# Kernel tuning notes

Measured on AMD Instinct MI355X. Metric: run time of the kernel, lower is better.

The kernel has to match this reference:

```python
import jax, jax.numpy as jnp
import numpy as np

B, S, H = 16, 2048, 1024


def setup_inputs() -> dict:
    key = jax.random.key(0)
    ks = jax.random.split(key, 8)
    scale = 1.0 / np.sqrt(H)
    return {
        "seq_embeddings": jax.random.normal(ks[0], (B, S, H), dtype=jnp.float32),
        "mask": jax.random.randint(ks[1], (B, S), 0, 2, dtype=jnp.int32),
        "Wq": jax.random.normal(ks[2], (H, H), dtype=jnp.float32) * scale,
        "bq": jnp.zeros((H,), dtype=jnp.float32),
        "Wk": jax.random.normal(ks[3], (H, H), dtype=jnp.float32) * scale,
        "bk": jnp.zeros((H,), dtype=jnp.float32),
        "Wv": jax.random.normal(ks[4], (H, H), dtype=jnp.float32) * scale,
        "bv": jnp.zeros((H,), dtype=jnp.float32),
    }


def reference(seq_embeddings, mask, Wq, bq, Wk, bk, Wv, bv):
    # Linear layers (torch convention: x @ W.T + b)
    Q = jnp.einsum("bsh,oh->bso", seq_embeddings, Wq) + bq
    K = jnp.einsum("bsh,oh->bso", seq_embeddings, Wk) + bk
    V = jnp.einsum("bsh,oh->bso", seq_embeddings, Wv) + bv

    inv_sqrt_d = 1.0 / jnp.sqrt(jnp.asarray(Q.shape[-1], Q.dtype))
    scores = jnp.einsum("bqh,bkh->bqk", Q, K) * inv_sqrt_d  # [B,S,S]
    # mask keys: mask[b,k]==0 -> -1e9 additive-equivalent fill
    scores = jnp.where(mask[:, None, :] == 0, jnp.asarray(-1e9, scores.dtype), scores)
    weights = jax.nn.softmax(scores, axis=-1)
    output = jnp.einsum("bqk,bkh->bqh", weights, V)
    # zero out padded query positions
    output = jnp.where(mask[:, :, None] == 0, jnp.asarray(0.0, output.dtype), output)
    return output
```

## Files before the change

### kernel.cpp

```cpp
#include <hip/hip_runtime.h>

#define Bn 16
#define Sn 2048
#define Hn 1024

typedef float floatx4 __attribute__((ext_vector_type(4)));
typedef __bf16 bf16x8 __attribute__((ext_vector_type(8)));
typedef unsigned short ushort8v __attribute__((ext_vector_type(8)));
typedef unsigned short ushort4v __attribute__((ext_vector_type(4)));

__device__ __forceinline__ unsigned short f2bf(float f) {
  unsigned u = __builtin_bit_cast(unsigned, f);
  u += 0x7FFFu + ((u >> 16) & 1u);
  return (unsigned short)(u >> 16);
}

__device__ __forceinline__ void async16(const unsigned short* g, unsigned short* l) {
  typedef __attribute__((address_space(1))) const unsigned char gu8;
  typedef __attribute__((address_space(3))) unsigned char lu8;
  __builtin_amdgcn_global_load_lds((gu8*)g, (lu8*)l, 16, 0, 0);
}

__device__ __forceinline__ void gemm256(const unsigned short* __restrict__ Ab,
                                        const unsigned short* __restrict__ Bb,
                                        int lda, int ldb, int K,
                                        unsigned short* lds, floatx4 acc[8][4]) {
  const int t = threadIdx.x;
  const int l = t & 63;
  const int w = t >> 6;
  const int srow = ((t >> 7) << 4) | (t & 15);
  const int sk = ((t >> 4) & 7) << 3;
  const int la = ((l >> 4) << 7) | ((l & 15) << 3);
  const int NT = K >> 6;
  const int wm = w >> 2, wn = w & 3;

#pragma unroll
  for (int i = 0; i < 8; ++i)
#pragma unroll
    for (int j = 0; j < 4; ++j)
#pragma unroll
      for (int e = 0; e < 4; ++e) acc[i][j][e] = 0.f;

#define STAGE(dstbase, srcp, ld, kk)                                     \
  {                                                                      \
    const unsigned short* _s = (srcp) + (size_t)srow * (ld) + (kk) + sk; \
    unsigned short* _d = (dstbase) + t * 8;                              \
    async16(_s, _d);                                                     \
    async16(_s + (size_t)64 * (ld), _d + 4096);                          \
  }

  {
    const int k1 = (NT > 1 ? 1 : 0) << 6;
    STAGE(lds + 0, Ab, lda, 0);
    STAGE(lds + 8192, Ab + (size_t)128 * lda, lda, 0);
    STAGE(lds + 16384, Bb, ldb, 0);
    STAGE(lds + 24576, Bb + (size_t)128 * ldb, ldb, 0);
    STAGE(lds + 32768 + 16384, Bb, ldb, k1);
    STAGE(lds + 32768 + 24576, Bb + (size_t)128 * ldb, ldb, k1);
  }
  asm volatile("s_waitcnt vmcnt(4)" ::: "memory");
  __builtin_amdgcn_s_barrier();
  __builtin_amdgcn_sched_barrier(0);

  bf16x8 aq[4][2], bA[2][2], bB[2][2];

  for (int tt = 0; tt < NT; ++tt) {
    unsigned short* bufc = lds + (tt & 1) * 32768;
    unsigned short* bufn = lds + ((tt & 1) ^ 1) * 32768;
    const unsigned short* As = bufc + wm * 8192;
    const unsigned short* Bs = bufc + 16384 + (wn >> 1) * 8192;
    const int cb = (wn & 1) * 4;
    const int kA = (tt + 1 < NT ? tt + 1 : 0) << 6;
    const int kB = (tt + 2 < NT ? tt + 2 : 0) << 6;

#pragma unroll
    for (int rf = 0; rf < 4; ++rf)
#pragma unroll
      for (int ks = 0; ks < 2; ++ks)
        aq[rf][ks] = *(const bf16x8*)(const void*)(As + rf * 1024 + ks * 512 + la);
#pragma unroll
    for (int cf = 0; cf < 2; ++cf)
#pragma unroll
      for (int ks = 0; ks < 2; ++ks)
        bA[cf][ks] = *(const bf16x8*)(const void*)(Bs + (cb + cf) * 1024 + ks * 512 + la);
    STAGE(bufn, Ab, lda, kA);
    __builtin_amdgcn_s_barrier();
    asm volatile("s_waitcnt lgkmcnt(0)" ::: "memory");
    __builtin_amdgcn_sched_barrier(0);
    __builtin_amdgcn_s_setprio(1);
#pragma unroll
    for (int rf = 0; rf < 4; ++rf)
#pragma unroll
      for (int cf = 0; cf < 2; ++cf)
#pragma unroll
        for (int ks = 0; ks < 2; ++ks)
          acc[rf][cf] = __builtin_amdgcn_mfma_f32_16x16x32_bf16(aq[rf][ks], bA[cf][ks], acc[rf][cf], 0, 0, 0);
    __builtin_amdgcn_s_setprio(0);
    __builtin_amdgcn_sched_barrier(0);
    __builtin_amdgcn_s_barrier();
    __builtin_amdgcn_sched_barrier(0);

#pragma unroll
    for (int cf = 0; cf < 2; ++cf)
#pragma unroll
      for (int ks = 0; ks < 2; ++ks)
        bB[cf][ks] = *(const bf16x8*)(const void*)(Bs + (cb + 2 + cf) * 1024 + ks * 512 + la);
    STAGE(bufn + 8192, Ab + (size_t)128 * lda, lda, kA);
    __builtin_amdgcn_s_barrier();
    asm volatile("s_waitcnt lgkmcnt(0)" ::: "memory");
    __builtin_amdgcn_sched_barrier(0);
    __builtin_amdgcn_s_setprio(1);
#pragma unroll
    for (int rf = 0; rf < 4; ++rf)
#pragma unroll
      for (int cf = 0; cf < 2; ++cf)
#pragma unroll
        for (int ks = 0; ks < 2; ++ks)
          acc[rf][2 + cf] = __builtin_amdgcn_mfma_f32_16x16x32_bf16(aq[rf][ks], bB[cf][ks], acc[rf][2 + cf], 0, 0, 0);
    __builtin_amdgcn_s_setprio(0);
    __builtin_amdgcn_sched_barrier(0);
    __builtin_amdgcn_s_barrier();
    __builtin_amdgcn_sched_barrier(0);

#pragma unroll
    for (int rf = 0; rf < 4; ++rf)
#pragma unroll
      for (int ks = 0; ks < 2; ++ks)
        aq[rf][ks] = *(const bf16x8*)(const void*)(As + (4 + rf) * 1024 + ks * 512 + la);
    STAGE(bufc + 16384, Bb, ldb, kB);
    __builtin_amdgcn_s_barrier();
    asm volatile("s_waitcnt lgkmcnt(0)" ::: "memory");
    __builtin_amdgcn_sched_barrier(0);
    __builtin_amdgcn_s_setprio(1);
#pragma unroll
    for (int rf = 0; rf < 4; ++rf)
#pragma unroll
      for (int cf = 0; cf < 2; ++cf)
#pragma unroll
        for (int ks = 0; ks < 2; ++ks)
          acc[4 + rf][2 + cf] = __builtin_amdgcn_mfma_f32_16x16x32_bf16(aq[rf][ks], bB[cf][ks], acc[4 + rf][2 + cf], 0, 0, 0);
    __builtin_amdgcn_s_setprio(0);
    __builtin_amdgcn_sched_barrier(0);
    __builtin_amdgcn_s_barrier();
    __builtin_amdgcn_sched_barrier(0);

    STAGE(bufc + 24576, Bb + (size_t)128 * ldb, ldb, kB);
    __builtin_amdgcn_s_barrier();
    __builtin_amdgcn_sched_barrier(0);
    __builtin_amdgcn_s_setprio(1);
#pragma unroll
    for (int rf = 0; rf < 4; ++rf)
#pragma unroll
      for (int cf = 0; cf < 2; ++cf)
#pragma unroll
        for (int ks = 0; ks < 2; ++ks)
          acc[4 + rf][cf] = __builtin_amdgcn_mfma_f32_16x16x32_bf16(aq[rf][ks], bA[cf][ks], acc[4 + rf][cf], 0, 0, 0);
    __builtin_amdgcn_s_setprio(0);
    asm volatile("s_waitcnt vmcnt(4)" ::: "memory");
    __builtin_amdgcn_sched_barrier(0);
    __builtin_amdgcn_s_barrier();
    __builtin_amdgcn_sched_barrier(0);
  }
  asm volatile("s_waitcnt vmcnt(0)" ::: "memory");
#undef STAGE
}

__global__ __launch_bounds__(256) void k_scan(const int* __restrict__ mask,
                                              int* __restrict__ act,
                                              int* __restrict__ cnt) {
  const int b = blockIdx.x;
  const int t = threadIdx.x;
  __shared__ int ps[256];
  const int* m = mask + b * Sn;
  int flags[8];
  int loc = 0;
#pragma unroll
  for (int i = 0; i < 8; ++i) {
    flags[i] = m[t * 8 + i] != 0;
    loc += flags[i];
  }
  ps[t] = loc;
  __syncthreads();
  for (int off = 1; off < 256; off <<= 1) {
    int v = (t >= off) ? ps[t - off] : 0;
    __syncthreads();
    ps[t] += v;
    __syncthreads();
  }
  int base = ps[t] - loc;
  int* ab = act + b * Sn;
#pragma unroll
  for (int i = 0; i < 8; ++i)
    if (flags[i]) ab[base++] = t * 8 + i;
  if (t == 255) {
    cnt[2 * b] = ps[255];
    cnt[2 * b + 1] = (ps[255] + 255) & ~255;
  }
}

__global__ __launch_bounds__(256) void k_cvt(const float* __restrict__ X,
                                             const float* __restrict__ Wq,
                                             const float* __restrict__ Wk,
                                             const float* __restrict__ Wv,
                                             const int* __restrict__ act,
                                             const int* __restrict__ cnt,
                                             unsigned short* __restrict__ Xc,
                                             unsigned short* __restrict__ Wb) {
  const size_t NW = (size_t)Hn * Hn;
  int blk = blockIdx.x;
  const int t = threadIdx.x;
  if (blk < 1536) {
    size_t j = (size_t)blk * 2048 + (size_t)t * 8;
    int wsel = (int)(j >> 20);
    size_t o = j & (NW - 1);
    const float* src = (wsel == 0 ? Wq : wsel == 1 ? Wk : Wv) + o;
    floatx4 a = __builtin_nontemporal_load((const floatx4*)src);
    floatx4 bdat = __builtin_nontemporal_load((const floatx4*)(src + 4));
    ushort8v o8;
    o8[0] = f2bf(a[0]); o8[1] = f2bf(a[1]); o8[2] = f2bf(a[2]); o8[3] = f2bf(a[3]);
    o8[4] = f2bf(bdat[0]); o8[5] = f2bf(bdat[1]); o8[6] = f2bf(bdat[2]); o8[7] = f2bf(bdat[3]);
    *(ushort8v*)(void*)(Wb + j) = o8;
    return;
  }
  blk -= 1536;
  const int b = blk >> 10;
  const int j = ((blk & 1023) << 1) | (t >> 7);
  if (j >= cnt[2 * b + 1]) return;
  const int c = (t & 127) * 8;
  unsigned short* dst = Xc + (size_t)(b * Sn + j) * Hn + c;
  if (j < cnt[2 * b]) {
    const int s = act[b * Sn + j];
    const float* src = X + (size_t)(b * Sn + s) * Hn + c;
    floatx4 a = __builtin_nontemporal_load((const floatx4*)src);
    floatx4 bdat = __builtin_nontemporal_load((const floatx4*)(src + 4));
    ushort8v o8;
    o8[0] = f2bf(a[0]); o8[1] = f2bf(a[1]); o8[2] = f2bf(a[2]); o8[3] = f2bf(a[3]);
    o8[4] = f2bf(bdat[0]); o8[5] = f2bf(bdat[1]); o8[6] = f2bf(bdat[2]); o8[7] = f2bf(bdat[3]);
    *(ushort8v*)(void*)(dst) = o8;
  } else {
    ushort8v z = {0, 0, 0, 0, 0, 0, 0, 0};
    *(ushort8v*)(void*)(dst) = z;
  }
}

__global__ __launch_bounds__(512, 2) void k_projall(const unsigned short* __restrict__ Xc,
                                                    const unsigned short* __restrict__ Wb,
                                                    const float* __restrict__ bq,
                                                    const float* __restrict__ bk,
                                                    const float* __restrict__ bv,
                                                    const int* __restrict__ cnt,
                                                    unsigned short* __restrict__ Qb,
                                                    unsigned short* __restrict__ Kb,
                                                    unsigned short* __restrict__ Vt) {
  __shared__ unsigned short lds[65536];
  const int b = blockIdx.z;
  const int mt = blockIdx.y * 256;
  if (mt >= cnt[2 * b + 1]) return;
  const int sel = blockIdx.x >> 2;
  const int n0 = (blockIdx.x & 3) * 256;
  const unsigned short* Ab = Xc + (size_t)(b * Sn + mt) * Hn;
  const unsigned short* Bbp = Wb + (size_t)sel * Hn * Hn + (size_t)n0 * Hn;
  floatx4 acc[8][4];
  gemm256(Ab, Bbp, Hn, Hn, Hn, lds, acc);

  const int t = threadIdx.x, l = t & 63, w = t >> 6;
  const int wm = w >> 2, wn = w & 3;
  const int q = l >> 4, c16 = l & 15;
  const float* bias = sel == 0 ? bq : sel == 1 ? bk : bv;

  if (sel < 2) {
    unsigned short* Out = sel == 0 ? Qb : Kb;
    const float oscale = sel == 0 ? 0.03125f : 1.0f;
#pragma unroll
    for (int cf = 0; cf < 4; ++cf) {
      const int col = n0 + wn * 64 + cf * 16 + c16;
      const float bb = bias[col];
#pragma unroll
      for (int rf = 0; rf < 8; ++rf) {
        const int row = b * Sn + mt + wm * 128 + rf * 16 + q * 4;
#pragma unroll
        for (int r = 0; r < 4; ++r)
          Out[(size_t)(row + r) * Hn + col] = f2bf((acc[rf][cf][r] + bb) * oscale);
      }
    }
  } else {
    const int s0 = mt + wm * 128;
    unsigned short* Vp = Vt + (size_t)b * Hn * Sn;
#pragma unroll
    for (int cf = 0; cf < 4; ++cf) {
      const int h = n0 + wn * 64 + cf * 16 + c16;
      const float bb = bias[h];
#pragma unroll
      for (int rf = 0; rf < 8; ++rf) {
        const int ss = s0 + rf * 16 + q * 4;
        ushort4v pk;
        pk[0] = f2bf(acc[rf][cf][0] + bb);
        pk[1] = f2bf(acc[rf][cf][1] + bb);
        pk[2] = f2bf(acc[rf][cf][2] + bb);
        pk[3] = f2bf(acc[rf][cf][3] + bb);
        __builtin_nontemporal_store(pk, (ushort4v*)(void*)(Vp + (size_t)h * Sn + ss));
      }
    }
  }
}

__global__ __launch_bounds__(512, 2) void k_scores(const unsigned short* __restrict__ Q,
                                                   const unsigned short* __restrict__ Kmat,
                                                   const int* __restrict__ cnt,
                                                   unsigned short* __restrict__ Sc,
                                                   float* __restrict__ Lsum) {
  __shared__ unsigned short lds[65536];
  const int b = blockIdx.z;
  const int cb = cnt[2 * b], cp = cnt[2 * b + 1];
  const int n0 = blockIdx.x * 256, m0 = blockIdx.y * 256;
  if (n0 >= cp || m0 >= cp) return;
  const unsigned short* Ab = Q + (size_t)(b * Sn + m0) * Hn;
  const unsigned short* Bbp = Kmat + (size_t)(b * Sn + n0) * Hn;
  floatx4 acc[8][4];
  gemm256(Ab, Bbp, Hn, Hn, Hn, lds, acc);

  const int t = threadIdx.x, l = t & 63, w = t >> 6;
  const int wm = w >> 2, wn = w & 3;
  const int q = l >> 4, c16 = l & 15;
  unsigned short* C = Sc + (size_t)b * Sn * Sn;
  float rs[8][4];
#pragma unroll
  for (int rf = 0; rf < 8; ++rf)
#pragma unroll
    for (int r = 0; r < 4; ++r) rs[rf][r] = 0.f;

#pragma unroll
  for (int cf = 0; cf < 4; ++cf) {
    const int col = n0 + wn * 64 + cf * 16 + c16;
    const bool mk = col < cb;
#pragma unroll
    for (int rf = 0; rf < 8; ++rf) {
      const int row = m0 + wm * 128 + rf * 16 + q * 4;
#pragma unroll
      for (int r = 0; r < 4; ++r) {
        const float e = mk ? __expf(acc[rf][cf][r]) : 0.f;
        C[(size_t)(row + r) * Sn + col] = f2bf(e);
        rs[rf][r] += e;
      }
    }
  }
#pragma unroll
  for (int rf = 0; rf < 8; ++rf)
#pragma unroll
    for (int r = 0; r < 4; ++r) {
      float v = rs[rf][r];
      v += __shfl_xor(v, 1);
      v += __shfl_xor(v, 2);
      v += __shfl_xor(v, 4);
      v += __shfl_xor(v, 8);
      rs[rf][r] = v;
    }
  if (c16 == 0) {
#pragma unroll
    for (int rf = 0; rf < 8; ++rf)
#pragma unroll
      for (int r = 0; r < 4; ++r)
        atomicAdd(&Lsum[b * Sn + m0 + wm * 128 + rf * 16 + q * 4 + r], rs[rf][r]);
  }
}

__global__ __launch_bounds__(512, 2) void k_out(const unsigned short* __restrict__ Wt,
                                                const unsigned short* __restrict__ Vt,
                                                const int* __restrict__ act,
                                                const int* __restrict__ cnt,
                                                const float* __restrict__ Lsum,
                                                float* __restrict__ Out) {
  __shared__ unsigned short lds[65536];
  const int b = blockIdx.z;
  const int cb = cnt[2 * b], cp = cnt[2 * b + 1];
  const int n0 = blockIdx.x * 256, m0 = blockIdx.y * 256;
  if (m0 >= cp) return;
  const unsigned short* Ab = Wt + (size_t)b * Sn * Sn + (size_t)m0 * Sn;
  const unsigned short* Bbp = Vt + (size_t)b * Hn * Sn + (size_t)n0 * Sn;
  floatx4 acc[8][4];
  gemm256(Ab, Bbp, Sn, Sn, cp, lds, acc);

  const int t = threadIdx.x, l = t & 63, w = t >> 6;
  const int wm = w >> 2, wn = w & 3;
  const int q = l >> 4, c16 = l & 15;
  float* C = Out + (size_t)b * Sn * Hn;
  const int* ab = act + b * Sn;
#pragma unroll
  for (int rf = 0; rf < 8; ++rf) {
    const int jb = m0 + wm * 128 + rf * 16 + q * 4;
    int srow[4];
    float inv[4];
    bool val[4];
#pragma unroll
    for (int r = 0; r < 4; ++r) {
      val[r] = (jb + r) < cb;
      srow[r] = val[r] ? ab[jb + r] : 0;
      inv[r] = val[r] ? 1.0f / Lsum[b * Sn + jb + r] : 0.f;
    }
#pragma unroll
    for (int cf = 0; cf < 4; ++cf) {
      const int col = n0 + wn * 64 + cf * 16 + c16;
#pragma unroll
      for (int r = 0; r < 4; ++r)
        if (val[r])
          __builtin_nontemporal_store(acc[rf][cf][r] * inv[r],
                                      &C[(size_t)srow[r] * Hn + col]);
    }
  }
}

extern "C" void kernel_launch(void* const* d_in, const int* in_sizes, int n_in,
                              void* d_out, int out_size, void* d_ws, size_t ws_size,
                              hipStream_t stream) {
  const float* X = (const float*)d_in[0];
  const int* mask = (const int*)d_in[1];
  const float* Wq = (const float*)d_in[2];
  const float* bq = (const float*)d_in[3];
  const float* Wk = (const float*)d_in[4];
  const float* bk = (const float*)d_in[5];
  const float* Wv = (const float*)d_in[6];
  const float* bv = (const float*)d_in[7];
  float* Out = (float*)d_out;

  const size_t NE = (size_t)Bn * Sn * Hn;
  const size_t NW = (size_t)Hn * Hn;
  unsigned short* Qb = (unsigned short*)d_ws;
  unsigned short* Kb = Qb + NE;
  unsigned short* Vt = Kb + NE;
  unsigned short* Sc = Vt + NE;
  unsigned short* Xc = Sc + (size_t)Bn * Sn * Sn;
  unsigned short* Wb = Xc + NE;
  int* act = (int*)(Wb + 3 * NW);
  int* cnt = act + (size_t)Bn * Sn;
  float* Lsum = (float*)Wb;

  k_scan<<<dim3(Bn, 1, 1), dim3(256, 1, 1), 0, stream>>>(mask, act, cnt);
  k_cvt<<<dim3(1536 + Bn * 1024, 1, 1), dim3(256, 1, 1), 0, stream>>>(
      X, Wq, Wk, Wv, act, cnt, Xc, Wb);
  hipMemsetAsync(Out, 0, (size_t)Bn * Sn * Hn * sizeof(float), stream);
  k_projall<<<dim3(12, Sn / 256, Bn), dim3(512, 1, 1), 0, stream>>>(
      Xc, Wb, bq, bk, bv, cnt, Qb, Kb, Vt);
  hipMemsetAsync(Lsum, 0, (size_t)Bn * Sn * sizeof(float), stream);
  k_scores<<<dim3(Sn / 256, Sn / 256, Bn), dim3(512, 1, 1), 0, stream>>>(
      Qb, Kb, cnt, Sc, Lsum);
  k_out<<<dim3(Hn / 256, Sn / 256, Bn), dim3(512, 1, 1), 0, stream>>>(
      Sc, Vt, act, cnt, Lsum, Out);
}
```

Baseline: 678.6 us.

## Swizzle LDS tile layout and remap block IDs for XCD-aware scheduling

Changes the shared-memory staging layout from a fragment-interleaved layout to row-major 64-wide rows with an XOR swizzle on the 16-byte chunk index. This is meant to keep global loads contiguous per row while avoiding LDS bank conflicts on the MFMA operand reads. It also remaps the flat block index in all three GEMM kernels so that consecutive blocks (which are distributed round-robin across the 8 XCDs) land on related tiles of the same batch, improving L2 reuse. The index arithmetic hardcodes the grid dimensions, and any swizzle mismatch would give wrong results.

```diff
diff --git a/kernel.cpp b/kernel.cpp
--- a/kernel.cpp
+++ b/kernel.cpp
@@ -28,11 +28,14 @@
   const int t = threadIdx.x;
   const int l = t & 63;
   const int w = t >> 6;
-  const int srow = ((t >> 7) << 4) | (t & 15);
-  const int sk = ((t >> 4) & 7) << 3;
-  const int la = ((l >> 4) << 7) | ((l & 15) << 3);
+  const int wm = w >> 2, wn = w & 3;
+  const int srow = t >> 3;
+  const int soff = ((t ^ (t >> 3)) & 7) << 3;
+  const int c16 = l & 15;
+  const int x0 = (((l >> 4) ^ l) & 7) << 3;
+  const int x1 = (((4 | (l >> 4)) ^ l) & 7) << 3;
+  const int cB = (wn & 1) * 64;
   const int NT = K >> 6;
-  const int wm = w >> 2, wn = w & 3;
 
 #pragma unroll
   for (int i = 0; i < 8; ++i)
@@ -41,12 +44,12 @@
 #pragma unroll
       for (int e = 0; e < 4; ++e) acc[i][j][e] = 0.f;
 
-#define STAGE(dstbase, srcp, ld, kk)                                     \
-  {                                                                      \
-    const unsigned short* _s = (srcp) + (size_t)srow * (ld) + (kk) + sk; \
-    unsigned short* _d = (dstbase) + t * 8;                              \
-    async16(_s, _d);                                                     \
-    async16(_s + (size_t)64 * (ld), _d + 4096);                          \
+#define STAGE(dstbase, srcp, ld, kk)                                      \
+  {                                                                       \
+    const unsigned short* _s = (srcp) + (size_t)srow * (ld) + (kk) + soff;\
+    unsigned short* _d = (dstbase) + t * 8;                               \
+    async16(_s, _d);                                                      \
+    async16(_s + (size_t)64 * (ld), _d + 4096);                           \
   }
 
   {
@@ -69,20 +72,19 @@
     unsigned short* bufn = lds + ((tt & 1) ^ 1) * 32768;
     const unsigned short* As = bufc + wm * 8192;
     const unsigned short* Bs = bufc + 16384 + (wn >> 1) * 8192;
-    const int cb = (wn & 1) * 4;
     const int kA = (tt + 1 < NT ? tt + 1 : 0) << 6;
     const int kB = (tt + 2 < NT ? tt + 2 : 0) << 6;
 
 #pragma unroll
-    for (int rf = 0; rf < 4; ++rf)
-#pragma unroll
-      for (int ks = 0; ks < 2; ++ks)
-        aq[rf][ks] = *(const bf16x8*)(const void*)(As + rf * 1024 + ks * 512 + la);
-#pragma unroll
-    for (int cf = 0; cf < 2; ++cf)
-#pragma unroll
-      for (int ks = 0; ks < 2; ++ks)
-        bA[cf][ks] = *(const bf16x8*)(const void*)(Bs + (cb + cf) * 1024 + ks * 512 + la);
+    for (int rf = 0; rf < 4; ++rf) {
+      aq[rf][0] = *(const bf16x8*)(const void*)(As + ((rf * 16 + c16) << 6) + x0);
+      aq[rf][1] = *(const bf16x8*)(const void*)(As + ((rf * 16 + c16) << 6) + x1);
+    }
+#pragma unroll
+    for (int cf = 0; cf < 2; ++cf) {
+      bA[cf][0] = *(const bf16x8*)(const void*)(Bs + ((cB + cf * 16 + c16) << 6) + x0);
+      bA[cf][1] = *(const bf16x8*)(const void*)(Bs + ((cB + cf * 16 + c16) << 6) + x1);
+    }
     STAGE(bufn, Ab, lda, kA);
     __builtin_amdgcn_s_barrier();
     asm volatile("s_waitcnt lgkmcnt(0)" ::: "memory");
@@ -101,10 +103,10 @@
     __builtin_amdgcn_sched_barrier(0);
 
 #pragma unroll
-    for (int cf = 0; cf < 2; ++cf)
-#pragma unroll
-      for (int ks = 0; ks < 2; ++ks)
-        bB[cf][ks] = *(const bf16x8*)(const void*)(Bs + (cb + 2 + cf) * 1024 + ks * 512 + la);
+    for (int cf = 0; cf < 2; ++cf) {
+      bB[cf][0] = *(const bf16x8*)(const void*)(Bs + ((cB + 32 + cf * 16 + c16) << 6) + x0);
+      bB[cf][1] = *(const bf16x8*)(const void*)(Bs + ((cB + 32 + cf * 16 + c16) << 6) + x1);
+    }
     STAGE(bufn + 8192, Ab + (size_t)128 * lda, lda, kA);
     __builtin_amdgcn_s_barrier();
     asm volatile("s_waitcnt lgkmcnt(0)" ::: "memory");
@@ -123,10 +125,10 @@
     __builtin_amdgcn_sched_barrier(0);
 
 #pragma unroll
-    for (int rf = 0; rf < 4; ++rf)
-#pragma unroll
-      for (int ks = 0; ks < 2; ++ks)
-        aq[rf][ks] = *(const bf16x8*)(const void*)(As + (4 + rf) * 1024 + ks * 512 + la);
+    for (int rf = 0; rf < 4; ++rf) {
+      aq[rf][0] = *(const bf16x8*)(const void*)(As + ((64 + rf * 16 + c16) << 6) + x0);
+      aq[rf][1] = *(const bf16x8*)(const void*)(As + ((64 + rf * 16 + c16) << 6) + x1);
+    }
     STAGE(bufc + 16384, Bb, ldb, kB);
     __builtin_amdgcn_s_barrier();
     asm volatile("s_waitcnt lgkmcnt(0)" ::: "memory");
@@ -253,11 +255,15 @@
                                                     unsigned short* __restrict__ Kb,
                                                     unsigned short* __restrict__ Vt) {
   __shared__ unsigned short lds[65536];
-  const int b = blockIdx.z;
-  const int mt = blockIdx.y * 256;
+  int flat = blockIdx.x + 12 * (blockIdx.y + 8 * blockIdx.z);
+  flat = (flat & 7) * 192 + (flat >> 3);
+  const int b = flat / 96;
+  int rem = flat - b * 96;
+  const int mt = (rem / 12) * 256;
+  rem -= (rem / 12) * 12;
+  const int sel = rem >> 2;
+  const int n0 = (rem & 3) * 256;
   if (mt >= cnt[2 * b + 1]) return;
-  const int sel = blockIdx.x >> 2;
-  const int n0 = (blockIdx.x & 3) * 256;
   const unsigned short* Ab = Xc + (size_t)(b * Sn + mt) * Hn;
   const unsigned short* Bbp = Wb + (size_t)sel * Hn * Hn + (size_t)n0 * Hn;
   floatx4 acc[8][4];
@@ -310,9 +316,12 @@
                                                    unsigned short* __restrict__ Sc,
                                                    float* __restrict__ Lsum) {
   __shared__ unsigned short lds[65536];
-  const int b = blockIdx.z;
+  int flat = blockIdx.x + 8 * (blockIdx.y + 8 * blockIdx.z);
+  flat = (flat & 7) * 128 + (flat >> 3);
+  const int b = flat >> 6;
+  const int m0 = ((flat >> 3) & 7) * 256;
+  const int n0 = (flat & 7) * 256;
   const int cb = cnt[2 * b], cp = cnt[2 * b + 1];
-  const int n0 = blockIdx.x * 256, m0 = blockIdx.y * 256;
   if (n0 >= cp || m0 >= cp) return;
   const unsigned short* Ab = Q + (size_t)(b * Sn + m0) * Hn;
   const unsigned short* Bbp = Kmat + (size_t)(b * Sn + n0) * Hn;
@@ -371,9 +380,12 @@
                                                 const float* __restrict__ Lsum,
                                                 float* __restrict__ Out) {
   __shared__ unsigned short lds[65536];
-  const int b = blockIdx.z;
+  int flat = blockIdx.x + 4 * (blockIdx.y + 8 * blockIdx.z);
+  flat = (flat & 7) * 64 + (flat >> 3);
+  const int b = flat >> 5;
+  const int m0 = ((flat >> 2) & 7) * 256;
+  const int n0 = (flat & 3) * 256;
   const int cb = cnt[2 * b], cp = cnt[2 * b + 1];
-  const int n0 = blockIdx.x * 256, m0 = blockIdx.y * 256;
   if (m0 >= cp) return;
   const unsigned short* Ab = Wt + (size_t)b * Sn * Sn + (size_t)m0 * Sn;
   const unsigned short* Bbp = Vt + (size_t)b * Hn * Sn + (size_t)n0 * Sn;
```

Result: faster. 571.9 us (-15.7%).
